# Optimization experiments

Measured on AMD Instinct MI355X. Metric: run time of the kernel, lower is better.

Reference implementation:

```python
import jax, jax.numpy as jnp
import numpy as np
from jax import lax

N, C1, C2, H, W = 4, 256, 256, 80, 80
CH = 128           # c_ = int(c2 * e)
G, KS = 1, 3       # groups, kernel_size
K = KS * KS        # sampling points per group
PAD, DIL = 1, 1
EPS_BN, EPS_LN = 1e-5, 1e-6


def conv_bn_silu(x, w, g, b, m, v, stride=1):
    # ultralytics Conv: conv(bias=False) + BatchNorm2d(eval) + SiLU
    pad = (w.shape[2] - 1) // 2
    y = lax.conv_general_dilated(x, w, (stride, stride), [(pad, pad), (pad, pad)],
                                 dimension_numbers=('NCHW', 'OIHW', 'NCHW'))
    s = g / jnp.sqrt(v + EPS_BN)
    y = y * s[None, :, None, None] + (b - m * s)[None, :, None, None]
    return jax.nn.silu(y)


def dcnv3_core(x, offset, mask):
    # x: (N,H,W,C) NHWC; offset: (N,H,W,G*K*2); mask: (N,H,W,G,K) softmaxed over K
    n, h, w, c = x.shape
    gc = c // G
    xp = jnp.pad(x, ((0, 0), (PAD, PAD), (PAD, PAD), (0, 0)))
    Hp, Wp = h + 2 * PAD, w + 2 * PAD
    base = (DIL * (KS - 1)) // 2
    # reference points (normalized by padded spatial size), stride 1
    ref_x = (jnp.arange(w, dtype=x.dtype) + base + 0.5) / Wp   # (W,)
    ref_y = (jnp.arange(h, dtype=x.dtype) + base + 0.5) / Hp   # (H,)
    gx = (jnp.arange(KS, dtype=x.dtype) * DIL - base) / Wp
    gy = (jnp.arange(KS, dtype=x.dtype) * DIL - base) / Hp
    grid_x = jnp.repeat(gx, KS)   # point p = i*KS + j -> x = gx[i]
    grid_y = jnp.tile(gy, KS)     # y = gy[j]  (torch meshgrid 'ij' ordering)
    off = offset.reshape(n, h, w, G, K, 2)
    loc_x = ref_x[None, None, :, None, None] + grid_x + off[..., 0] / Wp
    loc_y = ref_y[None, :, None, None, None] + grid_y + off[..., 1] / Hp
    # grid_sample align_corners=False: pixel = norm * size - 0.5
    px = loc_x * Wp - 0.5
    py = loc_y * Hp - 0.5
    x0 = jnp.floor(px); y0 = jnp.floor(py)
    lw, lh = px - x0, py - y0
    x0i, y0i = x0.astype(jnp.int32), y0.astype(jnp.int32)
    xv = jnp.transpose(xp.reshape(n, Hp * Wp, G, gc), (0, 2, 1, 3))  # (N,G,S,gc)
    tw = lambda a: jnp.transpose(a, (0, 3, 1, 2, 4))[..., None]      # (N,H,W,G,K)->(N,G,H,W,K,1)

    def gather(yi, xi):
        valid = ((xi >= 0) & (xi < Wp) & (yi >= 0) & (yi < Hp)).astype(x.dtype)
        idx = jnp.clip(yi, 0, Hp - 1) * Wp + jnp.clip(xi, 0, Wp - 1)
        idx = jnp.transpose(idx, (0, 3, 1, 2, 4)).reshape(n, G, h * w * K)
        v = jnp.take_along_axis(xv, idx[..., None], axis=2).reshape(n, G, h, w, K, gc)
        return v * tw(valid)   # zeros padding_mode

    out = (gather(y0i, x0i) * tw((1 - lh) * (1 - lw))
           + gather(y0i, x0i + 1) * tw((1 - lh) * lw)
           + gather(y0i + 1, x0i) * tw(lh * (1 - lw))
           + gather(y0i + 1, x0i + 1) * tw(lh * lw))   # (N,G,H,W,K,gc)
    m = jnp.transpose(mask, (0, 3, 1, 2, 4))[..., None]
    out = (out * m).sum(axis=4)                        # (N,G,H,W,gc)
    return jnp.transpose(out, (0, 2, 3, 1, 4)).reshape(n, h, w, c)


def forward(x, w1, g1, b1, m1, v1, w2, g2, b2, m2, v2,
            dw_w, dw_b, ln_g, ln_b, off_w, off_b, msk_w, msk_b,
            in_w, in_b, out_w, out_b, g3, b3, m3, v3):
    y = conv_bn_silu(x, w1, g1, b1, m1, v1)   # cv1: 3x3 Conv c1->c_
    y = conv_bn_silu(y, w2, g2, b2, m2, v2)   # cv2.conv: 1x1 Conv c_->c2
    t = jnp.transpose(y, (0, 2, 3, 1))        # NHWC
    x_proj = t @ in_w.T + in_b                # input_proj
    # dw_conv: depthwise 3x3 -> LayerNorm (channels_last) -> GELU
    dw = lax.conv_general_dilated(y, dw_w, (1, 1), [(1, 1), (1, 1)],
                                  dimension_numbers=('NCHW', 'OIHW', 'NCHW'),
                                  feature_group_count=C2)
    dw = jnp.transpose(dw, (0, 2, 3, 1)) + dw_b
    mu = dw.mean(-1, keepdims=True)
    var = ((dw - mu) ** 2).mean(-1, keepdims=True)
    dw = (dw - mu) / jnp.sqrt(var + EPS_LN) * ln_g + ln_b
    dw = jax.nn.gelu(dw, approximate=False)
    offset = dw @ off_w.T + off_b                                       # (N,H,W,G*K*2)
    mask = jax.nn.softmax((dw @ msk_w.T + msk_b).reshape(N, H, W, G, K), axis=-1)
    z = dcnv3_core(x_proj, offset, mask)
    z = z @ out_w.T + out_b                   # output_proj
    z = jnp.transpose(z, (0, 3, 1, 2))        # NCHW
    s = g3 / jnp.sqrt(v3 + EPS_BN)
    z = z * s[None, :, None, None] + (b3 - m3 * s)[None, :, None, None]
    z = jax.nn.silu(z)
    return x + z                              # shortcut (c1 == c2)


def setup_inputs():
    key = jax.random.key(0)
    ks = jax.random.split(key, 16)
    r = lambda k, s, sc=0.05: jax.random.normal(k, s, dtype=jnp.float32) * sc
    return {
        'x': jax.random.normal(ks[0], (N, C1, H, W), dtype=jnp.float32),
        'w1': r(ks[1], (CH, C1, 3, 3)),
        'g1': jnp.ones((CH,), jnp.float32), 'b1': jnp.zeros((CH,), jnp.float32),
        'm1': r(ks[2], (CH,), 0.1),
        'v1': jax.random.uniform(ks[3], (CH,), jnp.float32, 0.5, 1.5),
        'w2': r(ks[4], (C2, CH, 1, 1)),
        'g2': jnp.ones((C2,), jnp.float32), 'b2': jnp.zeros((C2,), jnp.float32),
        'm2': r(ks[5], (C2,), 0.1),
        'v2': jax.random.uniform(ks[6], (C2,), jnp.float32, 0.5, 1.5),
        'dw_w': r(ks[7], (C2, 1, 3, 3)), 'dw_b': jnp.zeros((C2,), jnp.float32),
        'ln_g': jnp.ones((C2,), jnp.float32), 'ln_b': jnp.zeros((C2,), jnp.float32),
        'off_w': r(ks[8], (G * K * 2, C2), 0.01), 'off_b': jnp.zeros((G * K * 2,), jnp.float32),
        'msk_w': r(ks[9], (G * K, C2), 0.01), 'msk_b': jnp.zeros((G * K,), jnp.float32),
        'in_w': r(ks[10], (C2, C2)), 'in_b': jnp.zeros((C2,), jnp.float32),
        'out_w': r(ks[11], (C2, C2)), 'out_b': jnp.zeros((C2,), jnp.float32),
        'g3': jnp.ones((C2,), jnp.float32), 'b3': jnp.zeros((C2,), jnp.float32),
        'm3': r(ks[12], (C2,), 0.1),
        'v3': jax.random.uniform(ks[13], (C2,), jnp.float32, 0.5, 1.5),
    }


def reference(x, w1, g1, b1, m1, v1, w2, g2, b2, m2, v2,
              dw_w, dw_b, ln_g, ln_b, off_w, off_b, msk_w, msk_b,
              in_w, in_b, out_w, out_b, g3, b3, m3, v3):
    return forward(x, w1, g1, b1, m1, v1, w2, g2, b2, m2, v2,
                   dw_w, dw_b, ln_g, ln_b, off_w, off_b, msk_w, msk_b,
                   in_w, in_b, out_w, out_b, g3, b3, m3, v3)
```

## Files before the change

### kernel.cpp

```cpp
#include <hip/hip_runtime.h>
#include <cmath>

#define TN 4
#define TC1 256
#define TCH 128
#define TC2 256
#define TH 80
#define TW 80
#define THP 82
#define TWP 84
#define NPIX (TN*TH*TW)

#define OFF_WBF   0
#define OFF_W2B   294912
#define OFF_INWB  327680
#define OFF_OUTWB 393216
#define OFF_DWT   458752
#define OFF_WCAT  461056
#define OFF_WCATB 467968
#define OFF_T1    468128
#define OFF_T2    468512
#define OFF_T3P   469024
#define OFF_XPAD  469504
#define OFF_Y1B   3997696
#define OFF_Y1P   7525888
#define OFF_Y2N   7525888
#define OFF_DWN   469504
#define OFF_RAWN  10802688
#define OFF_ZN    11493888

typedef __attribute__((ext_vector_type(8))) short bf16x8;
typedef __attribute__((ext_vector_type(4))) float f32x4;

__device__ __forceinline__ float siluf(float v) { return v / (1.f + expf(-v)); }
__device__ __forceinline__ short rnbf(float f) {
  unsigned u = __float_as_uint(f);
  unsigned r = (u + 0x7fffu + ((u >> 16) & 1u)) >> 16;
  return (short)r;
}
__device__ __forceinline__ float bf2f(short s) {
  return __uint_as_float(((unsigned)(unsigned short)s) << 16);
}

__global__ __launch_bounds__(256) void k_prep(
    const float* __restrict__ w1, const float* __restrict__ g1, const float* __restrict__ b1,
    const float* __restrict__ m1, const float* __restrict__ v1,
    const float* __restrict__ w2, const float* __restrict__ g2, const float* __restrict__ b2,
    const float* __restrict__ m2, const float* __restrict__ v2,
    const float* __restrict__ dww, const float* __restrict__ offw, const float* __restrict__ offb,
    const float* __restrict__ mskw, const float* __restrict__ mskb,
    const float* __restrict__ inw, const float* __restrict__ outw, const float* __restrict__ outb,
    const float* __restrict__ g3, const float* __restrict__ b3,
    const float* __restrict__ m3, const float* __restrict__ v3,
    float* __restrict__ ws)
{
  int i = blockIdx.x * 256 + threadIdx.x;
  if (i < 294912) {
    int co = i / 2304; int r = i - co * 2304;
    int tap = r >> 8; int ci = r & 255; int ky = tap / 3; int kx = tap - ky * 3;
    float s = g1[co] * __frsqrt_rn(v1[co] + 1e-5f);
    ((short*)(ws + OFF_WBF))[i] = rnbf(w1[((co * TC1 + ci) * 3 + ky) * 3 + kx] * s);
    return;
  }
  i -= 294912;
  if (i < 32768) {
    int co = i >> 7; int ci = i & 127;
    float s = g2[co] * __frsqrt_rn(v2[co] + 1e-5f);
    ((short*)(ws + OFF_W2B))[i] = rnbf(w2[co * TCH + ci] * s);
    return;
  }
  i -= 32768;
  if (i < 65536) {
    int co = i >> 8; int ci = i & 255;
    ((short*)(ws + OFF_INWB))[i] = rnbf(inw[co * TC2 + ci]);
    return;
  }
  i -= 65536;
  if (i < 65536) {
    int co = i >> 8; int ci = i & 255;
    float s = g3[co] * __frsqrt_rn(v3[co] + 1e-5f);
    ((short*)(ws + OFF_OUTWB))[i] = rnbf(outw[co * TC2 + ci] * s);
    return;
  }
  i -= 65536;
  if (i < 2304) { int c = i & 255; int j = i >> 8; ws[OFF_DWT + i] = dww[c * 9 + j]; return; }
  i -= 2304;
  if (i < 8192) {
    int c = i & 255; int j = i >> 8;
    float v = 0.f;
    if (j < 18) v = offw[j * 256 + c];
    else if (j < 27) v = mskw[(j - 18) * 256 + c];
    ((short*)(ws + OFF_WCAT))[i] = rnbf(v);
    return;
  }
  i -= 8192;
  if (i < 27) { ws[OFF_WCATB + i] = (i < 18) ? offb[i] : mskb[i - 18]; return; }
  i -= 27;
  if (i < 128) { float s = g1[i] / sqrtf(v1[i] + 1e-5f); ws[OFF_T1 + i] = b1[i] - m1[i] * s; return; }
  i -= 128;
  if (i < 256) { float s = g2[i] / sqrtf(v2[i] + 1e-5f); ws[OFF_T2 + i] = b2[i] - m2[i] * s; return; }
  i -= 256;
  if (i < 256) { float s = g3[i] / sqrtf(v3[i] + 1e-5f); ws[OFF_T3P + i] = outb[i] * s + b3[i] - m3[i] * s; return; }
}

__global__ __launch_bounds__(256) void k_padx(const float* __restrict__ x, short* __restrict__ xpn)
{
  __shared__ short lds[80 * 33];
  int b = blockIdx.x;
  int cc = b & 7; int hp = (b >> 3) % THP; int n = b / (THP * 8);
  int c0 = cc * 32;
  int t = threadIdx.x;
  int h = hp - 1;
  if (h >= 0 && h < TH) {
    for (int f = t; f < 80 * 32; f += 256) {
      int ci = f / 80; int w = f - ci * 80;
      lds[w * 33 + ci] = rnbf(x[((n * TC1 + c0 + ci) * TH + h) * TW + w]);
    }
  }
  __syncthreads();
  bool hv = (h >= 0 && h < TH);
  short* op = xpn + ((n * THP + hp) * TWP) * TC2 + c0;
  for (int g = t; g < TWP * 32; g += 256) {
    int ci = g & 31; int wp = g >> 5;
    short v = 0;
    if (hv && wp >= 1 && wp <= TW) v = lds[(wp - 1) * 33 + ci];
    op[wp * TC2 + ci] = v;
  }
}

#define A_STR 40
__global__ __launch_bounds__(256) void k_cv1(const short* __restrict__ xpn, const short* __restrict__ wbf,
                                             float* __restrict__ y1p)
{
  __shared__ short As[2][128 * A_STR];
  __shared__ short Bs[2][128 * A_STR];

  int b = blockIdx.x;
  int wt = b % 5; b /= 5; int ht = b % 10; b /= 10; int n = b & 3; int ks = b >> 2;
  int w0 = wt * 16, h0 = ht * 8;
  int tap0 = ks * 3;

  int tid = threadIdx.x;
  int wave = tid >> 6, lane = tid & 63;
  int ln = lane & 15, q = lane >> 4;
  int cohalf = (wave & 1) * 64;
  int pxhalf = (wave >> 1) * 64;

  int srow = tid >> 1;
  int ssub = (tid & 1) * 16;
  int hr = srow >> 4, wc = srow & 15;
  const short* arow = wbf + srow * 2304 + ssub;
  const short* brow = xpn + ((n * THP + h0 + hr) * TWP + (w0 + wc)) * 256 + ssub;

  f32x4 acc[4][4];
#pragma unroll
  for (int i = 0; i < 4; ++i)
#pragma unroll
    for (int j = 0; j < 4; ++j) acc[i][j] = (f32x4){0.f, 0.f, 0.f, 0.f};

  bf16x8 ra0, ra1, rb0, rb1;

  auto grab = [&](int c) {
    int rt = c >> 3;
    int atap = tap0 + rt;
    int ci0 = (c & 7) * 32;
    int ky = atap / 3, kx = atap - ky * 3;
    const short* ap = arow + atap * 256 + ci0;
    const short* bp = brow + (ky * TWP + kx) * 256 + ci0;
    ra0 = *(const bf16x8*)(ap);
    ra1 = *(const bf16x8*)(ap + 8);
    rb0 = *(const bf16x8*)(bp);
    rb1 = *(const bf16x8*)(bp + 8);
  };
  auto put = [&](int buf) {
    int o = srow * A_STR + ssub;
    *(bf16x8*)(&As[buf][o])     = ra0;
    *(bf16x8*)(&As[buf][o + 8]) = ra1;
    *(bf16x8*)(&Bs[buf][o])     = rb0;
    *(bf16x8*)(&Bs[buf][o + 8]) = rb1;
  };
  auto comp = [&](int buf) {
    bf16x8 af[4], bfv[4];
#pragma unroll
    for (int mt = 0; mt < 4; ++mt)
      af[mt] = *(const bf16x8*)(&As[buf][(cohalf + mt * 16 + ln) * A_STR + q * 8]);
#pragma unroll
    for (int nt = 0; nt < 4; ++nt)
      bfv[nt] = *(const bf16x8*)(&Bs[buf][(pxhalf + nt * 16 + ln) * A_STR + q * 8]);
#pragma unroll
    for (int mt = 0; mt < 4; ++mt)
#pragma unroll
      for (int nt = 0; nt < 4; ++nt)
        acc[mt][nt] = __builtin_amdgcn_mfma_f32_16x16x32_bf16(af[mt], bfv[nt], acc[mt][nt], 0, 0, 0);
  };

  grab(0);
  put(0);
  __syncthreads();
  for (int c = 0; c < 24; ++c) {
    if (c < 23) grab(c + 1);
    comp(c & 1);
    if (c < 23) {
      __syncthreads();
      put((c + 1) & 1);
      __syncthreads();
    }
  }

  float* yp = y1p + ks * (NPIX * TCH);
#pragma unroll
  for (int mt = 0; mt < 4; ++mt)
#pragma unroll
    for (int nt = 0; nt < 4; ++nt) {
      int p = pxhalf + nt * 16 + ln;
      int pr = p >> 4, pc = p & 15;
      int pix = (n * TH + h0 + pr) * TW + (w0 + pc);
      int co = cohalf + mt * 16 + q * 4;
      *(f32x4*)(yp + pix * TCH + co) = acc[mt][nt];
    }
}

__global__ __launch_bounds__(256) void k_y1red(const float* __restrict__ y1p, const float* __restrict__ t1v,
                                               short* __restrict__ y1b)
{
  int i = blockIdx.x * 256 + threadIdx.x;
  int co4 = (i & 31) * 4;
  int pix = i >> 5;
  float4 a = *(const float4*)(y1p + pix * TCH + co4);
  float4 bq = *(const float4*)(y1p + NPIX * TCH + pix * TCH + co4);
  float4 cq = *(const float4*)(y1p + 2 * NPIX * TCH + pix * TCH + co4);
  float4 t = *(const float4*)(t1v + co4);
  short4 o;
  o.x = rnbf(siluf(a.x + bq.x + cq.x + t.x));
  o.y = rnbf(siluf(a.y + bq.y + cq.y + t.y));
  o.z = rnbf(siluf(a.z + bq.z + cq.z + t.z));
  o.w = rnbf(siluf(a.w + bq.w + cq.w + t.w));
  *(short4*)(y1b + pix * TCH + co4) = o;
}

__global__ __launch_bounds__(256) void k_cv2(const short* __restrict__ y1b, const short* __restrict__ w2b,
                                             const float* __restrict__ t2v, short* __restrict__ y2b)
{
  int px0 = blockIdx.x * 32;
  int tid = threadIdx.x;
  int wave = tid >> 6, lane = tid & 63;
  int ln = lane & 15, q = lane >> 4;
  int co0 = wave * 64;
  int pix0 = px0 + ln;

  f32x4 acc[4][2];
#pragma unroll
  for (int mt = 0; mt < 4; ++mt)
#pragma unroll
    for (int pp = 0; pp < 2; ++pp) acc[mt][pp] = (f32x4){0.f, 0.f, 0.f, 0.f};

  const short* xb0 = y1b + pix0 * TCH + q * 8;
  const short* xb1 = xb0 + 16 * TCH;
  const short* wb = w2b + (co0 + ln) * TCH + q * 8;

  bf16x8 c0f = *(const bf16x8*)(xb0);
  bf16x8 c1f = *(const bf16x8*)(xb1);
  bf16x8 c2f = *(const bf16x8*)(wb + 0 * 16 * TCH);
  bf16x8 c3f = *(const bf16x8*)(wb + 1 * 16 * TCH);
  bf16x8 c4f = *(const bf16x8*)(wb + 2 * 16 * TCH);
  bf16x8 c5f = *(const bf16x8*)(wb + 3 * 16 * TCH);

#pragma unroll
  for (int kk = 0; kk < TCH; kk += 32) {
    bf16x8 n0f, n1f, n2f, n3f, n4f, n5f;
    const bool more = (kk + 32 < TCH);
    if (more) {
      n0f = *(const bf16x8*)(xb0 + kk + 32);
      n1f = *(const bf16x8*)(xb1 + kk + 32);
      n2f = *(const bf16x8*)(wb + 0 * 16 * TCH + kk + 32);
      n3f = *(const bf16x8*)(wb + 1 * 16 * TCH + kk + 32);
      n4f = *(const bf16x8*)(wb + 2 * 16 * TCH + kk + 32);
      n5f = *(const bf16x8*)(wb + 3 * 16 * TCH + kk + 32);
    }
    acc[0][0] = __builtin_amdgcn_mfma_f32_16x16x32_bf16(c2f, c0f, acc[0][0], 0, 0, 0);
    acc[0][1] = __builtin_amdgcn_mfma_f32_16x16x32_bf16(c2f, c1f, acc[0][1], 0, 0, 0);
    acc[1][0] = __builtin_amdgcn_mfma_f32_16x16x32_bf16(c3f, c0f, acc[1][0], 0, 0, 0);
    acc[1][1] = __builtin_amdgcn_mfma_f32_16x16x32_bf16(c3f, c1f, acc[1][1], 0, 0, 0);
    acc[2][0] = __builtin_amdgcn_mfma_f32_16x16x32_bf16(c4f, c0f, acc[2][0], 0, 0, 0);
    acc[2][1] = __builtin_amdgcn_mfma_f32_16x16x32_bf16(c4f, c1f, acc[2][1], 0, 0, 0);
    acc[3][0] = __builtin_amdgcn_mfma_f32_16x16x32_bf16(c5f, c0f, acc[3][0], 0, 0, 0);
    acc[3][1] = __builtin_amdgcn_mfma_f32_16x16x32_bf16(c5f, c1f, acc[3][1], 0, 0, 0);
    if (more) { c0f = n0f; c1f = n1f; c2f = n2f; c3f = n3f; c4f = n4f; c5f = n5f; }
  }

#pragma unroll
  for (int mt = 0; mt < 4; ++mt) {
    int co = co0 + mt * 16 + q * 4;
#pragma unroll
    for (int pp = 0; pp < 2; ++pp) {
      short4 p;
      p.x = rnbf(siluf(acc[mt][pp][0] + t2v[co]));
      p.y = rnbf(siluf(acc[mt][pp][1] + t2v[co + 1]));
      p.z = rnbf(siluf(acc[mt][pp][2] + t2v[co + 2]));
      p.w = rnbf(siluf(acc[mt][pp][3] + t2v[co + 3]));
      *(short4*)(y2b + (pix0 + pp * 16) * TC2 + co) = p;
    }
  }
}

__global__ __launch_bounds__(256) void k_proj_in(const short* __restrict__ y2b, const short* __restrict__ inwb,
                                                 const float* __restrict__ inb, short* __restrict__ xproj)
{
  int px0 = blockIdx.x * 32;
  int tid = threadIdx.x;
  int wave = tid >> 6, lane = tid & 63;
  int ln = lane & 15, q = lane >> 4;
  int co0 = wave * 64;
  int pix0 = px0 + ln;

  f32x4 acc[4][2];
#pragma unroll
  for (int mt = 0; mt < 4; ++mt)
#pragma unroll
    for (int pp = 0; pp < 2; ++pp) acc[mt][pp] = (f32x4){0.f, 0.f, 0.f, 0.f};

  const short* xb0 = y2b + pix0 * TC2 + q * 8;
  const short* xb1 = xb0 + 16 * TC2;
  const short* wb = inwb + (co0 + ln) * TC2 + q * 8;

  bf16x8 c0f = *(const bf16x8*)(xb0);
  bf16x8 c1f = *(const bf16x8*)(xb1);
  bf16x8 c2f = *(const bf16x8*)(wb + 0 * 16 * TC2);
  bf16x8 c3f = *(const bf16x8*)(wb + 1 * 16 * TC2);
  bf16x8 c4f = *(const bf16x8*)(wb + 2 * 16 * TC2);
  bf16x8 c5f = *(const bf16x8*)(wb + 3 * 16 * TC2);

#pragma unroll
  for (int kk = 0; kk < TC2; kk += 32) {
    bf16x8 n0f, n1f, n2f, n3f, n4f, n5f;
    const bool more = (kk + 32 < TC2);
    if (more) {
      n0f = *(const bf16x8*)(xb0 + kk + 32);
      n1f = *(const bf16x8*)(xb1 + kk + 32);
      n2f = *(const bf16x8*)(wb + 0 * 16 * TC2 + kk + 32);
      n3f = *(const bf16x8*)(wb + 1 * 16 * TC2 + kk + 32);
      n4f = *(const bf16x8*)(wb + 2 * 16 * TC2 + kk + 32);
      n5f = *(const bf16x8*)(wb + 3 * 16 * TC2 + kk + 32);
    }
    acc[0][0] = __builtin_amdgcn_mfma_f32_16x16x32_bf16(c2f, c0f, acc[0][0], 0, 0, 0);
    acc[0][1] = __builtin_amdgcn_mfma_f32_16x16x32_bf16(c2f, c1f, acc[0][1], 0, 0, 0);
    acc[1][0] = __builtin_amdgcn_mfma_f32_16x16x32_bf16(c3f, c0f, acc[1][0], 0, 0, 0);
    acc[1][1] = __builtin_amdgcn_mfma_f32_16x16x32_bf16(c3f, c1f, acc[1][1], 0, 0, 0);
    acc[2][0] = __builtin_amdgcn_mfma_f32_16x16x32_bf16(c4f, c0f, acc[2][0], 0, 0, 0);
    acc[2][1] = __builtin_amdgcn_mfma_f32_16x16x32_bf16(c4f, c1f, acc[2][1], 0, 0, 0);
    acc[3][0] = __builtin_amdgcn_mfma_f32_16x16x32_bf16(c5f, c0f, acc[3][0], 0, 0, 0);
    acc[3][1] = __builtin_amdgcn_mfma_f32_16x16x32_bf16(c5f, c1f, acc[3][1], 0, 0, 0);
    if (more) { c0f = n0f; c1f = n1f; c2f = n2f; c3f = n3f; c4f = n4f; c5f = n5f; }
  }

#pragma unroll
  for (int mt = 0; mt < 4; ++mt) {
    int co = co0 + mt * 16 + q * 4;
#pragma unroll
    for (int pp = 0; pp < 2; ++pp) {
      short4 p;
      p.x = rnbf(acc[mt][pp][0] + inb[co]);
      p.y = rnbf(acc[mt][pp][1] + inb[co + 1]);
      p.z = rnbf(acc[mt][pp][2] + inb[co + 2]);
      p.w = rnbf(acc[mt][pp][3] + inb[co + 3]);
      *(short4*)(xproj + (pix0 + pp * 16) * TC2 + co) = p;
    }
  }
}

__global__ __launch_bounds__(256) void k_dwln(const short* __restrict__ y2b, const float* __restrict__ dwt,
                                              const float* __restrict__ dwb, const float* __restrict__ lng,
                                              const float* __restrict__ lnb, short* __restrict__ dwo)
{
  int tid = threadIdx.x;
  int wave = tid >> 6, lane = tid & 63;
  int pix = blockIdx.x * 4 + wave;
  int w = pix % TW; int h = (pix / TW) % TH; int n = pix / (TH * TW);
  int c0 = lane * 4;

  float4 bb = *(const float4*)(dwb + c0);
  float v0 = bb.x, v1 = bb.y, v2 = bb.z, v3 = bb.w;
#pragma unroll
  for (int dy = 0; dy < 3; ++dy) {
    int hh = h + dy - 1;
    if (hh < 0 || hh >= TH) continue;
#pragma unroll
    for (int dx = 0; dx < 3; ++dx) {
      int ww = w + dx - 1;
      if (ww < 0 || ww >= TW) continue;
      short4 yv = *(const short4*)(y2b + ((n * TH + hh) * TW + ww) * TC2 + c0);
      float4 wv = *(const float4*)(dwt + (dy * 3 + dx) * TC2 + c0);
      v0 += bf2f(yv.x) * wv.x;
      v1 += bf2f(yv.y) * wv.y;
      v2 += bf2f(yv.z) * wv.z;
      v3 += bf2f(yv.w) * wv.w;
    }
  }
  float sv = v0 + v1 + v2 + v3;
  float sq = v0 * v0 + v1 * v1 + v2 * v2 + v3 * v3;
#pragma unroll
  for (int o = 32; o > 0; o >>= 1) { sv += __shfl_xor(sv, o); sq += __shfl_xor(sq, o); }
  float mu = sv * (1.f / 256.f);
  float var = sq * (1.f / 256.f) - mu * mu;
  float rs = 1.f / sqrtf(var + 1e-6f);
  float4 gv = *(const float4*)(lng + c0);
  float4 bv = *(const float4*)(lnb + c0);
  float n0 = (v0 - mu) * rs * gv.x + bv.x;
  float n1 = (v1 - mu) * rs * gv.y + bv.y;
  float n2 = (v2 - mu) * rs * gv.z + bv.z;
  float n3 = (v3 - mu) * rs * gv.w + bv.w;
  const float is2 = 0.70710678118654752f;
  short4 o4;
  o4.x = rnbf(0.5f * n0 * (1.f + erff(n0 * is2)));
  o4.y = rnbf(0.5f * n1 * (1.f + erff(n1 * is2)));
  o4.z = rnbf(0.5f * n2 * (1.f + erff(n2 * is2)));
  o4.w = rnbf(0.5f * n3 * (1.f + erff(n3 * is2)));
  *(short4*)(dwo + pix * TC2 + c0) = o4;
}

__global__ __launch_bounds__(256) void k_offmask(const short* __restrict__ dwo, const short* __restrict__ wcatb16,
                                                 const float* __restrict__ wcatb, float* __restrict__ raw)
{
  int tid = threadIdx.x;
  int wave = tid >> 6, lane = tid & 63;
  int ln = lane & 15, q = lane >> 4;
  int pix0 = blockIdx.x * 64 + wave * 16;

  f32x4 acc0 = {0.f, 0.f, 0.f, 0.f};
  f32x4 acc1 = acc0;

  const short* a0p = wcatb16 + ln * 256 + q * 8;
  const short* a1p = wcatb16 + (16 + ln) * 256 + q * 8;
  const short* bp  = dwo + (pix0 + ln) * 256 + q * 8;
#pragma unroll
  for (int kk = 0; kk < 256; kk += 32) {
    bf16x8 bf = *(const bf16x8*)(bp + kk);
    bf16x8 a0 = *(const bf16x8*)(a0p + kk);
    bf16x8 a1 = *(const bf16x8*)(a1p + kk);
    acc0 = __builtin_amdgcn_mfma_f32_16x16x32_bf16(a0, bf, acc0, 0, 0, 0);
    acc1 = __builtin_amdgcn_mfma_f32_16x16x32_bf16(a1, bf, acc1, 0, 0, 0);
  }

  int pix = pix0 + ln;
#pragma unroll
  for (int r = 0; r < 4; ++r) {
    int j0 = q * 4 + r;
    raw[pix * 27 + j0] = acc0[r] + wcatb[j0];
    int j1 = 16 + j0;
    if (j1 < 27) raw[pix * 27 + j1] = acc1[r] + wcatb[j1];
  }
}

__global__ __launch_bounds__(256) void k_dcn(const short* __restrict__ xproj, const float* __restrict__ raw,
                                             short* __restrict__ z)
{
  __shared__ int2 sp[4][36];
  int tid = threadIdx.x;
  int wave = tid >> 6, lane = tid & 63;
  int pix = blockIdx.x * 4 + wave;
  int w = pix % TW; int h = (pix / TW) % TH; int n = pix / (TH * TW);
  const float* r = raw + pix * 27;

  if (lane < 36) {
    int k = lane >> 2, tap = lane & 3;
    int tx = tap & 1, ty = tap >> 1;
    float mx = r[18];
#pragma unroll
    for (int kk = 1; kk < 9; ++kk) mx = fmaxf(mx, r[18 + kk]);
    float sum = 0.f, ek = 0.f;
#pragma unroll
    for (int kk = 0; kk < 9; ++kk) {
      float ee = expf(r[18 + kk] - mx);
      sum += ee;
      if (kk == k) ek = ee;
    }
    float mk = ek / sum;
    float px = (float)(w + k / 3) + r[2 * k];
    float py = (float)(h + k % 3) + r[2 * k + 1];
    float x0f = floorf(px), y0f = floorf(py);
    float lw = px - x0f, lh = py - y0f;
    int x0 = (int)x0f + tx, y0 = (int)y0f + ty;
    float wt = mk * (tx ? lw : 1.f - lw) * (ty ? lh : 1.f - lh);
    bool valid = (x0 >= 1) & (x0 <= TW) & (y0 >= 1) & (y0 <= TH);
    int2 pr;
    pr.x = valid ? (((y0 - 1) * TW + (x0 - 1)) * TC2) : 0;
    pr.y = valid ? __float_as_int(wt) : 0;
    sp[wave][lane] = pr;
  }
  __syncthreads();

  int c0 = lane * 4;
  const short* xb = xproj + n * (TH * TW * TC2) + c0;
  float a0 = 0.f, a1 = 0.f, a2 = 0.f, a3 = 0.f;
#pragma unroll
  for (int t = 0; t < 36; ++t) {
    int2 pr = sp[wave][t];
    float wt = __int_as_float(pr.y);
    short4 v = *(const short4*)(xb + pr.x);
    a0 += wt * bf2f(v.x);
    a1 += wt * bf2f(v.y);
    a2 += wt * bf2f(v.z);
    a3 += wt * bf2f(v.w);
  }
  short4 o;
  o.x = rnbf(a0); o.y = rnbf(a1); o.z = rnbf(a2); o.w = rnbf(a3);
  *(short4*)(z + pix * TC2 + c0) = o;
}

__global__ __launch_bounds__(256) void k_proj_out(const short* __restrict__ zb, const short* __restrict__ outwb,
                                                  const float* __restrict__ t3p,
                                                  const float* __restrict__ x, float* __restrict__ out)
{
  int px0 = blockIdx.x * 32;
  int tid = threadIdx.x;
  int wave = tid >> 6, lane = tid & 63;
  int ln = lane & 15, q = lane >> 4;
  int co0 = wave * 64;
  int pix0 = px0 + ln;

  f32x4 acc[4][2];
#pragma unroll
  for (int mt = 0; mt < 4; ++mt)
#pragma unroll
    for (int pp = 0; pp < 2; ++pp) acc[mt][pp] = (f32x4){0.f, 0.f, 0.f, 0.f};

  const short* xb0 = zb + pix0 * TC2 + q * 8;
  const short* xb1 = xb0 + 16 * TC2;
  const short* wb = outwb + (co0 + ln) * TC2 + q * 8;

  bf16x8 c0f = *(const bf16x8*)(xb0);
  bf16x8 c1f = *(const bf16x8*)(xb1);
  bf16x8 c2f = *(const bf16x8*)(wb + 0 * 16 * TC2);
  bf16x8 c3f = *(const bf16x8*)(wb + 1 * 16 * TC2);
  bf16x8 c4f = *(const bf16x8*)(wb + 2 * 16 * TC2);
  bf16x8 c5f = *(const bf16x8*)(wb + 3 * 16 * TC2);

#pragma unroll
  for (int kk = 0; kk < TC2; kk += 32) {
    bf16x8 n0f, n1f, n2f, n3f, n4f, n5f;
    const bool more = (kk + 32 < TC2);
    if (more) {
      n0f = *(const bf16x8*)(xb0 + kk + 32);
      n1f = *(const bf16x8*)(xb1 + kk + 32);
      n2f = *(const bf16x8*)(wb + 0 * 16 * TC2 + kk + 32);
      n3f = *(const bf16x8*)(wb + 1 * 16 * TC2 + kk + 32);
      n4f = *(const bf16x8*)(wb + 2 * 16 * TC2 + kk + 32);
      n5f = *(const bf16x8*)(wb + 3 * 16 * TC2 + kk + 32);
    }
    acc[0][0] = __builtin_amdgcn_mfma_f32_16x16x32_bf16(c2f, c0f, acc[0][0], 0, 0, 0);
    acc[0][1] = __builtin_amdgcn_mfma_f32_16x16x32_bf16(c2f, c1f, acc[0][1], 0, 0, 0);
    acc[1][0] = __builtin_amdgcn_mfma_f32_16x16x32_bf16(c3f, c0f, acc[1][0], 0, 0, 0);
    acc[1][1] = __builtin_amdgcn_mfma_f32_16x16x32_bf16(c3f, c1f, acc[1][1], 0, 0, 0);
    acc[2][0] = __builtin_amdgcn_mfma_f32_16x16x32_bf16(c4f, c0f, acc[2][0], 0, 0, 0);
    acc[2][1] = __builtin_amdgcn_mfma_f32_16x16x32_bf16(c4f, c1f, acc[2][1], 0, 0, 0);
    acc[3][0] = __builtin_amdgcn_mfma_f32_16x16x32_bf16(c5f, c0f, acc[3][0], 0, 0, 0);
    acc[3][1] = __builtin_amdgcn_mfma_f32_16x16x32_bf16(c5f, c1f, acc[3][1], 0, 0, 0);
    if (more) { c0f = n0f; c1f = n1f; c2f = n2f; c3f = n3f; c4f = n4f; c5f = n5f; }
  }

#pragma unroll
  for (int mt = 0; mt < 4; ++mt) {
#pragma unroll
    for (int pp = 0; pp < 2; ++pp) {
      int pix = pix0 + pp * 16;
      int n = pix / (TH * TW);
      int hw = pix - n * (TH * TW);
#pragma unroll
      for (int r = 0; r < 4; ++r) {
        int co = co0 + mt * 16 + q * 4 + r;
        int addr = (n * TC2 + co) * (TH * TW) + hw;
        out[addr] = x[addr] + siluf(acc[mt][pp][r] + t3p[co]);
      }
    }
  }
}

extern "C" void kernel_launch(void* const* d_in, const int* in_sizes, int n_in,
                              void* d_out, int out_size, void* d_ws, size_t ws_size,
                              hipStream_t stream)
{
  const float* x    = (const float*)d_in[0];
  const float* w1   = (const float*)d_in[1];
  const float* g1   = (const float*)d_in[2];
  const float* b1   = (const float*)d_in[3];
  const float* m1   = (const float*)d_in[4];
  const float* v1   = (const float*)d_in[5];
  const float* w2   = (const float*)d_in[6];
  const float* g2   = (const float*)d_in[7];
  const float* b2   = (const float*)d_in[8];
  const float* m2   = (const float*)d_in[9];
  const float* v2   = (const float*)d_in[10];
  const float* dww  = (const float*)d_in[11];
  const float* dwb  = (const float*)d_in[12];
  const float* lng  = (const float*)d_in[13];
  const float* lnb  = (const float*)d_in[14];
  const float* offw = (const float*)d_in[15];
  const float* offb = (const float*)d_in[16];
  const float* mskw = (const float*)d_in[17];
  const float* mskb = (const float*)d_in[18];
  const float* inw  = (const float*)d_in[19];
  const float* inb  = (const float*)d_in[20];
  const float* outw = (const float*)d_in[21];
  const float* outb = (const float*)d_in[22];
  const float* g3   = (const float*)d_in[23];
  const float* b3   = (const float*)d_in[24];
  const float* m3   = (const float*)d_in[25];
  const float* v3   = (const float*)d_in[26];

  float* ws  = (float*)d_ws;
  float* out = (float*)d_out;

  short* xpn    = (short*)(ws + OFF_XPAD);
  short* wbf    = (short*)(ws + OFF_WBF);
  short* w2b    = (short*)(ws + OFF_W2B);
  short* inwb   = (short*)(ws + OFF_INWB);
  short* outwb  = (short*)(ws + OFF_OUTWB);
  short* wcat16 = (short*)(ws + OFF_WCAT);
  float* y1p    = ws + OFF_Y1P;
  short* y1b    = (short*)(ws + OFF_Y1B);
  short* y2b    = (short*)(ws + OFF_Y2N);
  short* dwo    = (short*)(ws + OFF_DWN);
  float* raw    = ws + OFF_RAWN;
  short* zb     = (short*)(ws + OFF_ZN);
  short* xproj  = (short*)d_out;

  hipLaunchKernelGGL(k_prep, dim3(1836), dim3(256), 0, stream,
                     w1, g1, b1, m1, v1, w2, g2, b2, m2, v2,
                     dww, offw, offb, mskw, mskb, inw, outw, outb, g3, b3, m3, v3, ws);
  hipLaunchKernelGGL(k_padx,     dim3(TN * THP * 8), dim3(256), 0, stream, x, xpn);
  hipLaunchKernelGGL(k_cv1,      dim3(600),   dim3(256), 0, stream, xpn, wbf, y1p);
  hipLaunchKernelGGL(k_y1red,    dim3(3200),  dim3(256), 0, stream, y1p, ws + OFF_T1, y1b);
  hipLaunchKernelGGL(k_cv2,      dim3(800),   dim3(256), 0, stream, y1b, w2b, ws + OFF_T2, y2b);
  hipLaunchKernelGGL(k_proj_in,  dim3(800),   dim3(256), 0, stream, y2b, inwb, inb, xproj);
  hipLaunchKernelGGL(k_dwln,     dim3(6400),  dim3(256), 0, stream, y2b, ws + OFF_DWT, dwb, lng, lnb, dwo);
  hipLaunchKernelGGL(k_offmask,  dim3(400),   dim3(256), 0, stream, dwo, wcat16, ws + OFF_WCATB, raw);
  hipLaunchKernelGGL(k_dcn,      dim3(6400),  dim3(256), 0, stream, xproj, raw, zb);
  hipLaunchKernelGGL(k_proj_out, dim3(800),   dim3(256), 0, stream, zb, outwb, ws + OFF_T3P, x, out);
}
```

Before: 309.2 us.

## Tile 1x1-conv GEMMs as 128x128 LDS double-buffered blocks

Rewrites the three pointwise GEMM kernels (cv2, proj_in, proj_out) so each block computes a 128-channel by 128-pixel tile. A and B chunks are staged through double-buffered shared memory and each wave runs a 4x4 grid of MFMAs. Before, each wave loaded its operands straight from global memory for a 64x32 tile. This raises operand reuse and cuts redundant global and L2 traffic, at the cost of extra barriers, LDS usage, half as many blocks, and more accumulator registers. A_STR must be defined in the hidden part of the file.

```diff
diff --git a/kernel.cpp b/kernel.cpp
--- a/kernel.cpp
+++ b/kernel.cpp
@@ -241,64 +241,89 @@
 __global__ __launch_bounds__(256) void k_cv2(const short* __restrict__ y1b, const short* __restrict__ w2b,
                                              const float* __restrict__ t2v, short* __restrict__ y2b)
 {
-  int px0 = blockIdx.x * 32;
+  __shared__ short As[2][128 * A_STR];
+  __shared__ short Bs[2][128 * A_STR];
+
+  int b = blockIdx.x;
+  int ch = b & 1; int pt = b >> 1;
+  int co_base = ch * 128;
+  int pix0 = pt * 128;
+
   int tid = threadIdx.x;
   int wave = tid >> 6, lane = tid & 63;
   int ln = lane & 15, q = lane >> 4;
-  int co0 = wave * 64;
-  int pix0 = px0 + ln;
-
-  f32x4 acc[4][2];
-#pragma unroll
-  for (int mt = 0; mt < 4; ++mt)
-#pragma unroll
-    for (int pp = 0; pp < 2; ++pp) acc[mt][pp] = (f32x4){0.f, 0.f, 0.f, 0.f};
-
-  const short* xb0 = y1b + pix0 * TCH + q * 8;
-  const short* xb1 = xb0 + 16 * TCH;
-  const short* wb = w2b + (co0 + ln) * TCH + q * 8;
-
-  bf16x8 c0f = *(const bf16x8*)(xb0);
-  bf16x8 c1f = *(const bf16x8*)(xb1);
-  bf16x8 c2f = *(const bf16x8*)(wb + 0 * 16 * TCH);
-  bf16x8 c3f = *(const bf16x8*)(wb + 1 * 16 * TCH);
-  bf16x8 c4f = *(const bf16x8*)(wb + 2 * 16 * TCH);
-  bf16x8 c5f = *(const bf16x8*)(wb + 3 * 16 * TCH);
-
-#pragma unroll
-  for (int kk = 0; kk < TCH; kk += 32) {
-    bf16x8 n0f, n1f, n2f, n3f, n4f, n5f;
-    const bool more = (kk + 32 < TCH);
-    if (more) {
-      n0f = *(const bf16x8*)(xb0 + kk + 32);
-      n1f = *(const bf16x8*)(xb1 + kk + 32);
-      n2f = *(const bf16x8*)(wb + 0 * 16 * TCH + kk + 32);
-      n3f = *(const bf16x8*)(wb + 1 * 16 * TCH + kk + 32);
-      n4f = *(const bf16x8*)(wb + 2 * 16 * TCH + kk + 32);
-      n5f = *(const bf16x8*)(wb + 3 * 16 * TCH + kk + 32);
-    }
-    acc[0][0] = __builtin_amdgcn_mfma_f32_16x16x32_bf16(c2f, c0f, acc[0][0], 0, 0, 0);
-    acc[0][1] = __builtin_amdgcn_mfma_f32_16x16x32_bf16(c2f, c1f, acc[0][1], 0, 0, 0);
-    acc[1][0] = __builtin_amdgcn_mfma_f32_16x16x32_bf16(c3f, c0f, acc[1][0], 0, 0, 0);
-    acc[1][1] = __builtin_amdgcn_mfma_f32_16x16x32_bf16(c3f, c1f, acc[1][1], 0, 0, 0);
-    acc[2][0] = __builtin_amdgcn_mfma_f32_16x16x32_bf16(c4f, c0f, acc[2][0], 0, 0, 0);
-    acc[2][1] = __builtin_amdgcn_mfma_f32_16x16x32_bf16(c4f, c1f, acc[2][1], 0, 0, 0);
-    acc[3][0] = __builtin_amdgcn_mfma_f32_16x16x32_bf16(c5f, c0f, acc[3][0], 0, 0, 0);
-    acc[3][1] = __builtin_amdgcn_mfma_f32_16x16x32_bf16(c5f, c1f, acc[3][1], 0, 0, 0);
-    if (more) { c0f = n0f; c1f = n1f; c2f = n2f; c3f = n3f; c4f = n4f; c5f = n5f; }
+  int coh = (wave & 1) * 64;
+  int pxh = (wave >> 1) * 64;
+
+  int srow = tid >> 1;
+  int ssub = (tid & 1) * 16;
+  const short* arow = w2b + (co_base + srow) * TCH + ssub;
+  const short* brow = y1b + (pix0 + srow) * TCH + ssub;
+
+  f32x4 acc[4][4];
+#pragma unroll
+  for (int i = 0; i < 4; ++i)
+#pragma unroll
+    for (int j = 0; j < 4; ++j) acc[i][j] = (f32x4){0.f, 0.f, 0.f, 0.f};
+
+  bf16x8 ra0, ra1, rb0, rb1;
+  auto grab = [&](int c) {
+    const short* ap = arow + c * 32;
+    const short* bp = brow + c * 32;
+    ra0 = *(const bf16x8*)(ap);
+    ra1 = *(const bf16x8*)(ap + 8);
+    rb0 = *(const bf16x8*)(bp);
+    rb1 = *(const bf16x8*)(bp + 8);
+  };
+  auto put = [&](int buf) {
+    int o = srow * A_STR + ssub;
+    *(bf16x8*)(&As[buf][o])     = ra0;
+    *(bf16x8*)(&As[buf][o + 8]) = ra1;
+    *(bf16x8*)(&Bs[buf][o])     = rb0;
+    *(bf16x8*)(&Bs[buf][o + 8]) = rb1;
+  };
+  auto comp = [&](int buf) {
+    bf16x8 af[4], bfv[4];
+#pragma unroll
+    for (int mt = 0; mt < 4; ++mt)
+      af[mt] = *(const bf16x8*)(&As[buf][(coh + mt * 16 + ln) * A_STR + q * 8]);
+#pragma unroll
+    for (int nt = 0; nt < 4; ++nt)
+      bfv[nt] = *(const bf16x8*)(&Bs[buf][(pxh + nt * 16 + ln) * A_STR + q * 8]);
+#pragma unroll
+    for (int mt = 0; mt < 4; ++mt)
+#pragma unroll
+      for (int nt = 0; nt < 4; ++nt)
+        acc[mt][nt] = __builtin_amdgcn_mfma_f32_16x16x32_bf16(af[mt], bfv[nt], acc[mt][nt], 0, 0, 0);
+  };
+
+  const int NCH = TCH / 32;
+  grab(0);
+  put(0);
+  __syncthreads();
+  for (int c = 0; c < NCH; ++c) {
+    if (c < NCH - 1) grab(c + 1);
+    comp(c & 1);
+    if (c < NCH - 1) {
+      __syncthreads();
+      put((c + 1) & 1);
+      __syncthreads();
+    }
   }
 
 #pragma unroll
   for (int mt = 0; mt < 4; ++mt) {
-    int co = co0 + mt * 16 + q * 4;
-#pragma unroll
-    for (int pp = 0; pp < 2; ++pp) {
+    int co = co_base + coh + mt * 16 + q * 4;
+    float t0 = t2v[co], t1 = t2v[co + 1], t2 = t2v[co + 2], t3 = t2v[co + 3];
+#pragma unroll
+    for (int nt = 0; nt < 4; ++nt) {
+      int pix = pix0 + pxh + nt * 16 + ln;
       short4 p;
-      p.x = rnbf(siluf(acc[mt][pp][0] + t2v[co]));
-      p.y = rnbf(siluf(acc[mt][pp][1] + t2v[co + 1]));
-      p.z = rnbf(siluf(acc[mt][pp][2] + t2v[co + 2]));
-      p.w = rnbf(siluf(acc[mt][pp][3] + t2v[co + 3]));
-      *(short4*)(y2b + (pix0 + pp * 16) * TC2 + co) = p;
+      p.x = rnbf(siluf(acc[mt][nt][0] + t0));
+      p.y = rnbf(siluf(acc[mt][nt][1] + t1));
+      p.z = rnbf(siluf(acc[mt][nt][2] + t2));
+      p.w = rnbf(siluf(acc[mt][nt][3] + t3));
+      *(short4*)(y2b + pix * TC2 + co) = p;
     }
   }
 }
@@ -306,64 +331,89 @@
 __global__ __launch_bounds__(256) void k_proj_in(const short* __restrict__ y2b, const short* __restrict__ inwb,
                                                  const float* __restrict__ inb, short* __restrict__ xproj)
 {
-  int px0 = blockIdx.x * 32;
+  __shared__ short As[2][128 * A_STR];
+  __shared__ short Bs[2][128 * A_STR];
+
+  int b = blockIdx.x;
+  int ch = b & 1; int pt = b >> 1;
+  int co_base = ch * 128;
+  int pix0 = pt * 128;
+
   int tid = threadIdx.x;
   int wave = tid >> 6, lane = tid & 63;
   int ln = lane & 15, q = lane >> 4;
-  int co0 = wave * 64;
-  int pix0 = px0 + ln;
-
-  f32x4 acc[4][2];
-#pragma unroll
-  for (int mt = 0; mt < 4; ++mt)
-#pragma unroll
-    for (int pp = 0; pp < 2; ++pp) acc[mt][pp] = (f32x4){0.f, 0.f, 0.f, 0.f};
-
-  const short* xb0 = y2b + pix0 * TC2 + q * 8;
-  const short* xb1 = xb0 + 16 * TC2;
-  const short* wb = inwb + (co0 + ln) * TC2 + q * 8;
-
-  bf16x8 c0f = *(const bf16x8*)(xb0);
-  bf16x8 c1f = *(const bf16x8*)(xb1);
-  bf16x8 c2f = *(const bf16x8*)(wb + 0 * 16 * TC2);
-  bf16x8 c3f = *(const bf16x8*)(wb + 1 * 16 * TC2);
-  bf16x8 c4f = *(const bf16x8*)(wb + 2 * 16 * TC2);
-  bf16x8 c5f = *(const bf16x8*)(wb + 3 * 16 * TC2);
-
-#pragma unroll
-  for (int kk = 0; kk < TC2; kk += 32) {
-    bf16x8 n0f, n1f, n2f, n3f, n4f, n5f;
-    const bool more = (kk + 32 < TC2);
-    if (more) {
-      n0f = *(const bf16x8*)(xb0 + kk + 32);
-      n1f = *(const bf16x8*)(xb1 + kk + 32);
-      n2f = *(const bf16x8*)(wb + 0 * 16 * TC2 + kk + 32);
-      n3f = *(const bf16x8*)(wb + 1 * 16 * TC2 + kk + 32);
-      n4f = *(const bf16x8*)(wb + 2 * 16 * TC2 + kk + 32);
-      n5f = *(const bf16x8*)(wb + 3 * 16 * TC2 + kk + 32);
-    }
-    acc[0][0] = __builtin_amdgcn_mfma_f32_16x16x32_bf16(c2f, c0f, acc[0][0], 0, 0, 0);
-    acc[0][1] = __builtin_amdgcn_mfma_f32_16x16x32_bf16(c2f, c1f, acc[0][1], 0, 0, 0);
-    acc[1][0] = __builtin_amdgcn_mfma_f32_16x16x32_bf16(c3f, c0f, acc[1][0], 0, 0, 0);
-    acc[1][1] = __builtin_amdgcn_mfma_f32_16x16x32_bf16(c3f, c1f, acc[1][1], 0, 0, 0);
-    acc[2][0] = __builtin_amdgcn_mfma_f32_16x16x32_bf16(c4f, c0f, acc[2][0], 0, 0, 0);
-    acc[2][1] = __builtin_amdgcn_mfma_f32_16x16x32_bf16(c4f, c1f, acc[2][1], 0, 0, 0);
-    acc[3][0] = __builtin_amdgcn_mfma_f32_16x16x32_bf16(c5f, c0f, acc[3][0], 0, 0, 0);
-    acc[3][1] = __builtin_amdgcn_mfma_f32_16x16x32_bf16(c5f, c1f, acc[3][1], 0, 0, 0);
-    if (more) { c0f = n0f; c1f = n1f; c2f = n2f; c3f = n3f; c4f = n4f; c5f = n5f; }
+  int coh = (wave & 1) * 64;
+  int pxh = (wave >> 1) * 64;
+
+  int srow = tid >> 1;
+  int ssub = (tid & 1) * 16;
+  const short* arow = inwb + (co_base + srow) * TC2 + ssub;
+  const short* brow = y2b + (pix0 + srow) * TC2 + ssub;
+
+  f32x4 acc[4][4];
+#pragma unroll
+  for (int i = 0; i < 4; ++i)
+#pragma unroll
+    for (int j = 0; j < 4; ++j) acc[i][j] = (f32x4){0.f, 0.f, 0.f, 0.f};
+
+  bf16x8 ra0, ra1, rb0, rb1;
+  auto grab = [&](int c) {
+    const short* ap = arow + c * 32;
+    const short* bp = brow + c * 32;
+    ra0 = *(const bf16x8*)(ap);
+    ra1 = *(const bf16x8*)(ap + 8);
+    rb0 = *(const bf16x8*)(bp);
+    rb1 = *(const bf16x8*)(bp + 8);
+  };
+  auto put = [&](int buf) {
+    int o = srow * A_STR + ssub;
+    *(bf16x8*)(&As[buf][o])     = ra0;
+    *(bf16x8*)(&As[buf][o + 8]) = ra1;
+    *(bf16x8*)(&Bs[buf][o])     = rb0;
+    *(bf16x8*)(&Bs[buf][o + 8]) = rb1;
+  };
+  auto comp = [&](int buf) {
+    bf16x8 af[4], bfv[4];
+#pragma unroll
+    for (int mt = 0; mt < 4; ++mt)
+      af[mt] = *(const bf16x8*)(&As[buf][(coh + mt * 16 + ln) * A_STR + q * 8]);
+#pragma unroll
+    for (int nt = 0; nt < 4; ++nt)
+      bfv[nt] = *(const bf16x8*)(&Bs[buf][(pxh + nt * 16 + ln) * A_STR + q * 8]);
+#pragma unroll
+    for (int mt = 0; mt < 4; ++mt)
+#pragma unroll
+      for (int nt = 0; nt < 4; ++nt)
+        acc[mt][nt] = __builtin_amdgcn_mfma_f32_16x16x32_bf16(af[mt], bfv[nt], acc[mt][nt], 0, 0, 0);
+  };
+
+  const int NCH = TC2 / 32;
+  grab(0);
+  put(0);
+  __syncthreads();
+  for (int c = 0; c < NCH; ++c) {
+    if (c < NCH - 1) grab(c + 1);
+    comp(c & 1);
+    if (c < NCH - 1) {
+      __syncthreads();
+      put((c + 1) & 1);
+      __syncthreads();
+    }
   }
 
 #pragma unroll
   for (int mt = 0; mt < 4; ++mt) {
-    int co = co0 + mt * 16 + q * 4;
-#pragma unroll
-    for (int pp = 0; pp < 2; ++pp) {
+    int co = co_base + coh + mt * 16 + q * 4;
+    float b0 = inb[co], b1 = inb[co + 1], b2 = inb[co + 2], b3 = inb[co + 3];
+#pragma unroll
+    for (int nt = 0; nt < 4; ++nt) {
+      int pix = pix0 + pxh + nt * 16 + ln;
       short4 p;
-      p.x = rnbf(acc[mt][pp][0] + inb[co]);
-      p.y = rnbf(acc[mt][pp][1] + inb[co + 1]);
-      p.z = rnbf(acc[mt][pp][2] + inb[co + 2]);
-      p.w = rnbf(acc[mt][pp][3] + inb[co + 3]);
-      *(short4*)(xproj + (pix0 + pp * 16) * TC2 + co) = p;
+      p.x = rnbf(acc[mt][nt][0] + b0);
+      p.y = rnbf(acc[mt][nt][1] + b1);
+      p.z = rnbf(acc[mt][nt][2] + b2);
+      p.w = rnbf(acc[mt][nt][3] + b3);
+      *(short4*)(xproj + pix * TC2 + co) = p;
     }
   }
 }
@@ -511,65 +561,88 @@
                                                   const float* __restrict__ t3p,
                                                   const float* __restrict__ x, float* __restrict__ out)
 {
-  int px0 = blockIdx.x * 32;
+  __shared__ short As[2][128 * A_STR];
+  __shared__ short Bs[2][128 * A_STR];
+
+  int b = blockIdx.x;
+  int ch = b & 1; int pt = b >> 1;
+  int co_base = ch * 128;
+  int pix0 = pt * 128;
+
   int tid = threadIdx.x;
   int wave = tid >> 6, lane = tid & 63;
   int ln = lane & 15, q = lane >> 4;
-  int co0 = wave * 64;
-  int pix0 = px0 + ln;
-
-  f32x4 acc[4][2];
-#pragma unroll
-  for (int mt = 0; mt < 4; ++mt)
-#pragma unroll
-    for (int pp = 0; pp < 2; ++pp) acc[mt][pp] = (f32x4){0.f, 0.f, 0.f, 0.f};
-
-  const short* xb0 = zb + pix0 * TC2 + q * 8;
-  const short* xb1 = xb0 + 16 * TC2;
-  const short* wb = outwb + (co0 + ln) * TC2 + q * 8;
-
-  bf16x8 c0f = *(const bf16x8*)(xb0);
-  bf16x8 c1f = *(const bf16x8*)(xb1);
-  bf16x8 c2f = *(const bf16x8*)(wb + 0 * 16 * TC2);
-  bf16x8 c3f = *(const bf16x8*)(wb + 1 * 16 * TC2);
-  bf16x8 c4f = *(const bf16x8*)(wb + 2 * 16 * TC2);
-  bf16x8 c5f = *(const bf16x8*)(wb + 3 * 16 * TC2);
-
-#pragma unroll
-  for (int kk = 0; kk < TC2; kk += 32) {
-    bf16x8 n0f, n1f, n2f, n3f, n4f, n5f;
-    const bool more = (kk + 32 < TC2);
-    if (more) {
-      n0f = *(const bf16x8*)(xb0 + kk + 32);
-      n1f = *(const bf16x8*)(xb1 + kk + 32);
-      n2f = *(const bf16x8*)(wb + 0 * 16 * TC2 + kk + 32);
-      n3f = *(const bf16x8*)(wb + 1 * 16 * TC2 + kk + 32);
-      n4f = *(const bf16x8*)(wb + 2 * 16 * TC2 + kk + 32);
-      n5f = *(const bf16x8*)(wb + 3 * 16 * TC2 + kk + 32);
-    }
-    acc[0][0] = __builtin_amdgcn_mfma_f32_16x16x32_bf16(c2f, c0f, acc[0][0], 0, 0, 0);
-    acc[0][1] = __builtin_amdgcn_mfma_f32_16x16x32_bf16(c2f, c1f, acc[0][1], 0, 0, 0);
-    acc[1][0] = __builtin_amdgcn_mfma_f32_16x16x32_bf16(c3f, c0f, acc[1][0], 0, 0, 0);
-    acc[1][1] = __builtin_amdgcn_mfma_f32_16x16x32_bf16(c3f, c1f, acc[1][1], 0, 0, 0);
-    acc[2][0] = __builtin_amdgcn_mfma_f32_16x16x32_bf16(c4f, c0f, acc[2][0], 0, 0, 0);
-    acc[2][1] = __builtin_amdgcn_mfma_f32_16x16x32_bf16(c4f, c1f, acc[2][1], 0, 0, 0);
-    acc[3][0] = __builtin_amdgcn_mfma_f32_16x16x32_bf16(c5f, c0f, acc[3][0], 0, 0, 0);
-    acc[3][1] = __builtin_amdgcn_mfma_f32_16x16x32_bf16(c5f, c1f, acc[3][1], 0, 0, 0);
-    if (more) { c0f = n0f; c1f = n1f; c2f = n2f; c3f = n3f; c4f = n4f; c5f = n5f; }
+  int coh = (wave & 1) * 64;
+  int pxh = (wave >> 1) * 64;
+
+  int srow = tid >> 1;
+  int ssub = (tid & 1) * 16;
+  const short* arow = outwb + (co_base + srow) * TC2 + ssub;
+  const short* brow = zb + (pix0 + srow) * TC2 + ssub;
+
+  f32x4 acc[4][4];
+#pragma unroll
+  for (int i = 0; i < 4; ++i)
+#pragma unroll
+    for (int j = 0; j < 4; ++j) acc[i][j] = (f32x4){0.f, 0.f, 0.f, 0.f};
+
+  bf16x8 ra0, ra1, rb0, rb1;
+  auto grab = [&](int c) {
+    const short* ap = arow + c * 32;
+    const short* bp = brow + c * 32;
+    ra0 = *(const bf16x8*)(ap);
+    ra1 = *(const bf16x8*)(ap + 8);
+    rb0 = *(const bf16x8*)(bp);
+    rb1 = *(const bf16x8*)(bp + 8);
+  };
+  auto put = [&](int buf) {
+    int o = srow * A_STR + ssub;
+    *(bf16x8*)(&As[buf][o])     = ra0;
+    *(bf16x8*)(&As[buf][o + 8]) = ra1;
+    *(bf16x8*)(&Bs[buf][o])     = rb0;
+    *(bf16x8*)(&Bs[buf][o + 8]) = rb1;
+  };
+  auto comp = [&](int buf) {
+    bf16x8 af[4], bfv[4];
+#pragma unroll
+    for (int mt = 0; mt < 4; ++mt)
+      af[mt] = *(const bf16x8*)(&As[buf][(coh + mt * 16 + ln) * A_STR + q * 8]);
+#pragma unroll
+    for (int nt = 0; nt < 4; ++nt)
+      bfv[nt] = *(const bf16x8*)(&Bs[buf][(pxh + nt * 16 + ln) * A_STR + q * 8]);
+#pragma unroll
+    for (int mt = 0; mt < 4; ++mt)
+#pragma unroll
+      for (int nt = 0; nt < 4; ++nt)
+        acc[mt][nt] = __builtin_amdgcn_mfma_f32_16x16x32_bf16(af[mt], bfv[nt], acc[mt][nt], 0, 0, 0);
+  };
+
+  const int NCH = TC2 / 32;
+  grab(0);
+  put(0);
+  __syncthreads();
+  for (int c = 0; c < NCH; ++c) {
+    if (c < NCH - 1) grab(c + 1);
+    comp(c & 1);
+    if (c < NCH - 1) {
+      __syncthreads();
+      put((c + 1) & 1);
+      __syncthreads();
+    }
   }
 
 #pragma unroll
   for (int mt = 0; mt < 4; ++mt) {
-#pragma unroll
-    for (int pp = 0; pp < 2; ++pp) {
-      int pix = pix0 + pp * 16;
+    int co = co_base + coh + mt * 16 + q * 4;
+#pragma unroll
+    for (int nt = 0; nt < 4; ++nt) {
+      int pix = pix0 + pxh + nt * 16 + ln;
       int n = pix / (TH * TW);
       int hw = pix - n * (TH * TW);
 #pragma unroll
       for (int r = 0; r < 4; ++r) {
-        int co = co0 + mt * 16 + q * 4 + r;
-        int addr = (n * TC2 + co) * (TH * TW) + hw;
-        out[addr] = x[addr] + siluf(acc[mt][pp][r] + t3p[co]);
+        int addr = (n * TC2 + co + r) * (TH * TW) + hw;
+        out[addr] = x[addr] + siluf(acc[mt][nt][r] + t3p[co + r]);
       }
     }
   }
@@ -630,10 +703,10 @@
   hipLaunchKernelGGL(k_padx,     dim3(TN * THP * 8), dim3(256), 0, stream, x, xpn);
   hipLaunchKernelGGL(k_cv1,      dim3(600),   dim3(256), 0, stream, xpn, wbf, y1p);
   hipLaunchKernelGGL(k_y1red,    dim3(3200),  dim3(256), 0, stream, y1p, ws + OFF_T1, y1b);
-  hipLaunchKernelGGL(k_cv2,      dim3(800),   dim3(256), 0, stream, y1b, w2b, ws + OFF_T2, y2b);
-  hipLaunchKernelGGL(k_proj_in,  dim3(800),   dim3(256), 0, stream, y2b, inwb, inb, xproj);
+  hipLaunchKernelGGL(k_cv2,      dim3(400),   dim3(256), 0, stream, y1b, w2b, ws + OFF_T2, y2b);
+  hipLaunchKernelGGL(k_proj_in,  dim3(400),   dim3(256), 0, stream, y2b, inwb, inb, xproj);
   hipLaunchKernelGGL(k_dwln,     dim3(6400),  dim3(256), 0, stream, y2b, ws + OFF_DWT, dwb, lng, lnb, dwo);
   hipLaunchKernelGGL(k_offmask,  dim3(400),   dim3(256), 0, stream, dwo, wcat16, ws + OFF_WCATB, raw);
   hipLaunchKernelGGL(k_dcn,      dim3(6400),  dim3(256), 0, stream, xproj, raw, zb);
-  hipLaunchKernelGGL(k_proj_out, dim3(800),   dim3(256), 0, stream, zb, outwb, ws + OFF_T3P, x, out);
-}
+  hipLaunchKernelGGL(k_proj_out, dim3(400),   dim3(256), 0, stream, zb, outwb, ws + OFF_T3P, x, out);
+}
```

New measurement: 294.4 us. 4.8% less time.
